# Kernel tuning notes

Measured on AMD Instinct MI355X. Metric: run time of the kernel, lower is better.

The kernel has to match this reference:

```python
import jax, jax.numpy as jnp
import numpy as np
import itertools

SKS = 3
GROUPS = 8
PAD = (SKS - 1) // 2


def setup_inputs() -> dict:
    key = jax.random.key(0)
    k1, k2 = jax.random.split(key)
    B, C, D, H, W = 2, 64, 64, 64, 64
    x = jax.random.normal(k1, (B, C, D, H, W), dtype=jnp.float32)
    w = jax.random.normal(k2, (B, GROUPS, SKS ** 3, D, H, W), dtype=jnp.float32)
    return {"x": x, "w": w}


def reference(x, w):
    # x: [B, C, D, H, W]; w: [B, G, sks^3, D, H, W]
    B, C, D, H, W = x.shape
    G = GROUPS
    # group the channels: [B, G, C//G, D, H, W]
    xg = x.reshape(B, G, C // G, D, H, W)
    offsets = list(itertools.product(range(-PAD, PAD + 1), repeat=3))  # (di, hi, wi), 27 taps
    out = jnp.zeros_like(xg)
    for k, (di, hi, wi) in enumerate(offsets):
        # circular shift matching torch.roll(x_g, (-di,-hi,-wi), dims=(2,3,4))
        shifted = jnp.roll(xg, shift=(-di, -hi, -wi), axis=(3, 4, 5))
        # broadcast per-group dynamic weight over the C//G channels in the group
        out = out + shifted * w[:, :, k][:, :, None]  # [B,G,C//G,D,H,W]
    return out.reshape(B, C, D, H, W)
```

## Files before the change

kernel.cpp:

```cpp
#include <hip/hip_runtime.h>


#define ND 64
#define NH 64
#define NW 64
#define HW 4096
#define DHW 262144
#define CPG 8

typedef const __attribute__((address_space(1))) unsigned int* gp_as1;
typedef __attribute__((address_space(3))) unsigned int* lp_as3;

__global__ __launch_bounds__(64, 1) void ska3d_kernel(const float* __restrict__ x,
                                                      const float* __restrict__ w,
                                                      float* __restrict__ out) {
    __shared__ float lds[4][CPG][6][NW];

    const int lane = threadIdx.x;
    const int w0   = (lane & 15) * 4;
    const int hl   = lane >> 4;

    const int bid = blockIdx.x;
    const int dc  = bid & 7;
    const int ht  = (bid >> 3) & 15;
    const int g   = (bid >> 7) & 7;
    const int b   = bid >> 10;

    const int d0 = dc * 8;
    const int h0 = ht * 4;
    const int h  = h0 + hl;

    const float* xb = x + (size_t)(b * 64 + g * CPG) * DHW;
    const float* wb = w + (size_t)(b * 8 + g) * 27 * DHW;
    float* ob = out + (size_t)(b * 64 + g * CPG) * DHW + h * NW + w0;

    const int wlb = (w0 + 60) & 63;
    const int wrb = (w0 + 4) & 63;

#define STAGE(p) do {                                                          \
        const int slot_ = (p) & 3;                                             \
        const int dd_   = (p) & 63;                                            \
        _Pragma("unroll")                                                      \
        for (int i = 0; i < 12; ++i) {                                         \
            const int fid = i * 64 + lane;            \
            const int c_  = fid / 96;               \
            const int rm_ = fid - c_ * 96;                                     \
            const int r_  = rm_ >> 4;                                \
            const int ws_ = rm_ & 15;                               \
            const int hh_ = (h0 - 1 + r_) & 63;                                \
            const float* gsrc = xb + (size_t)c_ * DHW + dd_ * HW + hh_ * NW + ws_ * 4; \
            __builtin_amdgcn_global_load_lds((gp_as1)gsrc,                     \
                (lp_as3)&lds[slot_][c_][r_][ws_ * 4], 16, 0, 0);               \
        }                                                                      \
    } while (0)

    STAGE(d0 - 1);
    STAGE(d0);
    STAGE(d0 + 1);
    asm volatile("s_waitcnt vmcnt(0)" ::: "memory");

    for (int d = d0; d < d0 + 8; ++d) {
        STAGE(d + 2);

        float4 wk[27];
        const float* wpd = wb + (size_t)d * HW + h * NW + w0;
#pragma unroll
        for (int k = 0; k < 27; ++k)
            wk[k] = *(const float4*)(wpd + (size_t)k * DHW);

        asm volatile("s_waitcnt vmcnt(47)" ::: "memory");

        float acc[CPG][4];
#pragma unroll
        for (int c = 0; c < CPG; ++c)
            acc[c][0] = acc[c][1] = acc[c][2] = acc[c][3] = 0.f;

#pragma unroll
        for (int di = -1; di <= 1; ++di) {
            const int slot = (d + di) & 3;
#pragma unroll
            for (int hi = -1; hi <= 1; ++hi) {
                const int r  = hl + hi + 1;
                const int kb = (di + 1) * 9 + (hi + 1) * 3;
#pragma unroll
                for (int c = 0; c < CPG; ++c) {
                    const float* row = &lds[slot][c][r][0];
                    const float4 xm = *(const float4*)(row + wlb);
                    const float4 xv = *(const float4*)(row + w0);
                    const float4 xp = *(const float4*)(row + wrb);
                    const float4 wa = wk[kb], wm = wk[kb + 1], wc = wk[kb + 2];
                    acc[c][0] += wa.x * xm.w;  acc[c][1] += wa.y * xv.x;
                    acc[c][2] += wa.z * xv.y;  acc[c][3] += wa.w * xv.z;
                    acc[c][0] += wm.x * xv.x;  acc[c][1] += wm.y * xv.y;
                    acc[c][2] += wm.z * xv.z;  acc[c][3] += wm.w * xv.w;
                    acc[c][0] += wc.x * xv.y;  acc[c][1] += wc.y * xv.z;
                    acc[c][2] += wc.z * xv.w;  acc[c][3] += wc.w * xp.x;
                }
            }
        }

#pragma unroll
        for (int c = 0; c < CPG; ++c)
            *(float4*)(ob + (size_t)c * DHW + (size_t)d * HW) =
                make_float4(acc[c][0], acc[c][1], acc[c][2], acc[c][3]);
    }
}

extern "C" void kernel_launch(void* const* d_in, const int* in_sizes, int n_in,
                              void* d_out, int out_size, void* d_ws, size_t ws_size,
                              hipStream_t stream) {
    const float* x = (const float*)d_in[0];
    const float* w = (const float*)d_in[1];
    float* out = (float*)d_out;
    dim3 grid(2048);
    dim3 block(64);
    hipLaunchKernelGGL(ska3d_kernel, grid, block, 0, stream, x, w, out);
}
```

Baseline: 178.6 us.

## Double-buffer per-depth weight loads one slice ahead and shrink halo LDS reads

The depth loop is unrolled with two register sets for the 27 weight float4s. The weights for slice d+1 are issued while slice d is computed, so global weight latency overlaps with the FMA work instead of stalling at the start of each iteration. The left and right halo reads from LDS become single scalar loads instead of float4 loads, which cuts LDS traffic. In exchange, register pressure roughly doubles for the weights, and the manual vmcnt accounting becomes more fragile.

```diff
diff --git a/kernel.cpp b/kernel.cpp
--- a/kernel.cpp
+++ b/kernel.cpp
@@ -31,11 +31,11 @@
     const int h  = h0 + hl;
 
     const float* xb = x + (size_t)(b * 64 + g * CPG) * DHW;
-    const float* wb = w + (size_t)(b * 8 + g) * 27 * DHW;
+    const float* wb = w + (size_t)(b * 8 + g) * 27 * DHW + h * NW + w0;
     float* ob = out + (size_t)(b * 64 + g * CPG) * DHW + h * NW + w0;
 
-    const int wlb = (w0 + 60) & 63;
-    const int wrb = (w0 + 4) & 63;
+    const int wl = (w0 + 63) & 63;
+    const int wr = (w0 + 4) & 63;
 
 #define STAGE(p) do {                                                          \
         const int slot_ = (p) & 3;                                             \
@@ -43,7 +43,7 @@
         _Pragma("unroll")                                                      \
         for (int i = 0; i < 12; ++i) {                                         \
             const int fid = i * 64 + lane;            \
-            const int c_  = fid / 96;               \
+            const int c_  = fid / 96;                                          \
             const int rm_ = fid - c_ * 96;                                     \
             const int r_  = rm_ >> 4;                                \
             const int ws_ = rm_ & 15;                               \
@@ -54,56 +54,71 @@
         }                                                                      \
     } while (0)
 
+#define LOADW(arr, dp) do {                                                    \
+        const float* wpn_ = wb + (size_t)(dp) * HW;                            \
+        _Pragma("unroll")                                                      \
+        for (int k = 0; k < 27; ++k)                                           \
+            arr[k] = *(const float4*)(wpn_ + (size_t)k * DHW);                 \
+    } while (0)
+
+#define COMPUTE(d, WK) do {                                                    \
+        float acc[CPG][4];                                                     \
+        _Pragma("unroll")                                                      \
+        for (int c = 0; c < CPG; ++c)                                          \
+            acc[c][0] = acc[c][1] = acc[c][2] = acc[c][3] = 0.f;               \
+        _Pragma("unroll")                                                      \
+        for (int di = -1; di <= 1; ++di) {                                     \
+            const int slot = ((d) + di) & 3;                                   \
+            _Pragma("unroll")                                                  \
+            for (int hi = -1; hi <= 1; ++hi) {                                 \
+                const int r  = hl + hi + 1;                                    \
+                const int kb = (di + 1) * 9 + (hi + 1) * 3;                    \
+                _Pragma("unroll")                                              \
+                for (int c = 0; c < CPG; ++c) {                                \
+                    const float* row = &lds[slot][c][r][0];                    \
+                    const float  xm = row[wl];                                 \
+                    const float4 xv = *(const float4*)(row + w0);              \
+                    const float  xp = row[wr];                                 \
+                    const float4 wa = WK[kb], wm = WK[kb + 1], wc = WK[kb + 2];\
+                    acc[c][0] += wa.x * xm;    acc[c][1] += wa.y * xv.x;       \
+                    acc[c][2] += wa.z * xv.y;  acc[c][3] += wa.w * xv.z;       \
+                    acc[c][0] += wm.x * xv.x;  acc[c][1] += wm.y * xv.y;       \
+                    acc[c][2] += wm.z * xv.z;  acc[c][3] += wm.w * xv.w;       \
+                    acc[c][0] += wc.x * xv.y;  acc[c][1] += wc.y * xv.z;       \
+                    acc[c][2] += wc.z * xv.w;  acc[c][3] += wc.w * xp;         \
+                }                                                              \
+            }                                                                  \
+        }                                                                      \
+        _Pragma("unroll")                                                      \
+        for (int c = 0; c < CPG; ++c)                                          \
+            *(float4*)(ob + (size_t)c * DHW + (size_t)(d) * HW) =              \
+                make_float4(acc[c][0], acc[c][1], acc[c][2], acc[c][3]);       \
+    } while (0)
+
+#define BODY(d, WC, WN) do {                                                   \
+        STAGE((d) + 2);                                                        \
+        LOADW(WN, (d) + 1);                                                    \
+        asm volatile("s_waitcnt vmcnt(47)" ::: "memory");                      \
+        COMPUTE((d), WC);                                                      \
+    } while (0)
+
+    float4 wkA[27], wkB[27];
+
     STAGE(d0 - 1);
     STAGE(d0);
     STAGE(d0 + 1);
+    LOADW(wkA, d0);
     asm volatile("s_waitcnt vmcnt(0)" ::: "memory");
 
-    for (int d = d0; d < d0 + 8; ++d) {
-        STAGE(d + 2);
+#pragma unroll
+    for (int i = 0; i < 3; ++i) {
+        BODY(d0 + 2 * i,     wkA, wkB);
+        BODY(d0 + 2 * i + 1, wkB, wkA);
+    }
+    BODY(d0 + 6, wkA, wkB);
 
-        float4 wk[27];
-        const float* wpd = wb + (size_t)d * HW + h * NW + w0;
-#pragma unroll
-        for (int k = 0; k < 27; ++k)
-            wk[k] = *(const float4*)(wpd + (size_t)k * DHW);
-
-        asm volatile("s_waitcnt vmcnt(47)" ::: "memory");
-
-        float acc[CPG][4];
-#pragma unroll
-        for (int c = 0; c < CPG; ++c)
-            acc[c][0] = acc[c][1] = acc[c][2] = acc[c][3] = 0.f;
-
-#pragma unroll
-        for (int di = -1; di <= 1; ++di) {
-            const int slot = (d + di) & 3;
-#pragma unroll
-            for (int hi = -1; hi <= 1; ++hi) {
-                const int r  = hl + hi + 1;
-                const int kb = (di + 1) * 9 + (hi + 1) * 3;
-#pragma unroll
-                for (int c = 0; c < CPG; ++c) {
-                    const float* row = &lds[slot][c][r][0];
-                    const float4 xm = *(const float4*)(row + wlb);
-                    const float4 xv = *(const float4*)(row + w0);
-                    const float4 xp = *(const float4*)(row + wrb);
-                    const float4 wa = wk[kb], wm = wk[kb + 1], wc = wk[kb + 2];
-                    acc[c][0] += wa.x * xm.w;  acc[c][1] += wa.y * xv.x;
-                    acc[c][2] += wa.z * xv.y;  acc[c][3] += wa.w * xv.z;
-                    acc[c][0] += wm.x * xv.x;  acc[c][1] += wm.y * xv.y;
-                    acc[c][2] += wm.z * xv.z;  acc[c][3] += wm.w * xv.w;
-                    acc[c][0] += wc.x * xv.y;  acc[c][1] += wc.y * xv.z;
-                    acc[c][2] += wc.z * xv.w;  acc[c][3] += wc.w * xp.x;
-                }
-            }
-        }
-
-#pragma unroll
-        for (int c = 0; c < CPG; ++c)
-            *(float4*)(ob + (size_t)c * DHW + (size_t)d * HW) =
-                make_float4(acc[c][0], acc[c][1], acc[c][2], acc[c][3]);
-    }
+    asm volatile("s_waitcnt vmcnt(8)" ::: "memory");
+    COMPUTE(d0 + 7, wkB);
 }
 
 extern "C" void kernel_launch(void* const* d_in, const int* in_sizes, int n_in,
```

Result: slower. 182.3 us (+2.1%).

## Split group channels across four waves per block and prefetch next-depth weights

Applied to the files above, without the earlier changes.

Each block grows from one wave to four. Each wave computes two of the group's eight channels, and the three LDS halo planes are staged cooperatively, with an explicit s_waitcnt plus s_barrier per depth step. The 27 dynamic-weight vectors for the next depth slice are now loaded right after the current slice's stores, so their latency overlaps the next barrier and staging instead of sitting in front of the compute. The aim is more waves in flight to hide memory latency, and fewer registers per wave. In exchange, all four waves fetch the same weights, so per-block weight requests rise four-fold and depend on cache hits, and the new barrier adds a sync cost.

```diff
diff --git a/kernel.cpp b/kernel.cpp
--- a/kernel.cpp
+++ b/kernel.cpp
@@ -6,19 +6,21 @@
 #define NW 64
 #define HW 4096
 #define DHW 262144
-#define CPG 8
 
 typedef const __attribute__((address_space(1))) unsigned int* gp_as1;
 typedef __attribute__((address_space(3))) unsigned int* lp_as3;
 
-__global__ __launch_bounds__(64, 1) void ska3d_kernel(const float* __restrict__ x,
-                                                      const float* __restrict__ w,
-                                                      float* __restrict__ out) {
-    __shared__ float lds[4][CPG][6][NW];
+__global__ __launch_bounds__(256, 2) void ska3d_kernel(const float* __restrict__ x,
+                                                       const float* __restrict__ w,
+                                                       float* __restrict__ out) {
+    __shared__ float lds[4][8][6][NW];
 
-    const int lane = threadIdx.x;
+    const int tid  = threadIdx.x;
+    const int lane = tid & 63;
+    const int wv   = tid >> 6;
     const int w0   = (lane & 15) * 4;
     const int hl   = lane >> 4;
+    const int c0   = wv * 2;
 
     const int bid = blockIdx.x;
     const int dc  = bid & 7;
@@ -30,20 +32,20 @@
     const int h0 = ht * 4;
     const int h  = h0 + hl;
 
-    const float* xb = x + (size_t)(b * 64 + g * CPG) * DHW;
-    const float* wb = w + (size_t)(b * 8 + g) * 27 * DHW;
-    float* ob = out + (size_t)(b * 64 + g * CPG) * DHW + h * NW + w0;
+    const float* xb = x + (size_t)(b * 64 + g * 8) * DHW;
+    const float* wb = w + (size_t)(b * 8 + g) * 27 * DHW + h * NW + w0;
+    float* ob = out + (size_t)(b * 64 + g * 8 + c0) * DHW + h * NW + w0;
 
-    const int wlb = (w0 + 60) & 63;
-    const int wrb = (w0 + 4) & 63;
+    const int wl = (w0 + 63) & 63;
+    const int wr = (w0 + 4) & 63;
 
 #define STAGE(p) do {                                                          \
         const int slot_ = (p) & 3;                                             \
         const int dd_   = (p) & 63;                                            \
         _Pragma("unroll")                                                      \
-        for (int i = 0; i < 12; ++i) {                                         \
-            const int fid = i * 64 + lane;            \
-            const int c_  = fid / 96;               \
+        for (int i = 0; i < 3; ++i) {                                          \
+            const int fid = i * 256 + tid;                         \
+            const int c_  = fid / 96;                                          \
             const int rm_ = fid - c_ * 96;                                     \
             const int r_  = rm_ >> 4;                                \
             const int ws_ = rm_ & 15;                               \
@@ -54,26 +56,34 @@
         }                                                                      \
     } while (0)
 
+#define LOADW(dp) do {                                                         \
+        const float* wpn_ = wb + (size_t)(dp) * HW;                            \
+        _Pragma("unroll")                                                      \
+        for (int k = 0; k < 27; ++k)                                           \
+            wk[k] = *(const float4*)(wpn_ + (size_t)k * DHW);                  \
+    } while (0)
+
+    float4 wk[27];
+
     STAGE(d0 - 1);
     STAGE(d0);
     STAGE(d0 + 1);
+    LOADW(d0);
     asm volatile("s_waitcnt vmcnt(0)" ::: "memory");
 
-    for (int d = d0; d < d0 + 8; ++d) {
-        STAGE(d + 2);
+#pragma unroll 1
+    for (int i = 0; i < 8; ++i) {
+        const int d = d0 + i;
 
-        float4 wk[27];
-        const float* wpd = wb + (size_t)d * HW + h * NW + w0;
+        asm volatile("s_waitcnt vmcnt(29)" ::: "memory");
+        asm volatile("s_barrier" ::: "memory");
+
+        if (i < 7) STAGE(d + 2);
+
+        float acc[2][4];
 #pragma unroll
-        for (int k = 0; k < 27; ++k)
-            wk[k] = *(const float4*)(wpd + (size_t)k * DHW);
-
-        asm volatile("s_waitcnt vmcnt(47)" ::: "memory");
-
-        float acc[CPG][4];
-#pragma unroll
-        for (int c = 0; c < CPG; ++c)
-            acc[c][0] = acc[c][1] = acc[c][2] = acc[c][3] = 0.f;
+        for (int cc = 0; cc < 2; ++cc)
+            acc[cc][0] = acc[cc][1] = acc[cc][2] = acc[cc][3] = 0.f;
 
 #pragma unroll
         for (int di = -1; di <= 1; ++di) {
@@ -83,26 +93,28 @@
                 const int r  = hl + hi + 1;
                 const int kb = (di + 1) * 9 + (hi + 1) * 3;
 #pragma unroll
-                for (int c = 0; c < CPG; ++c) {
-                    const float* row = &lds[slot][c][r][0];
-                    const float4 xm = *(const float4*)(row + wlb);
+                for (int cc = 0; cc < 2; ++cc) {
+                    const float* row = &lds[slot][c0 + cc][r][0];
+                    const float  xm = row[wl];
                     const float4 xv = *(const float4*)(row + w0);
-                    const float4 xp = *(const float4*)(row + wrb);
+                    const float  xp = row[wr];
                     const float4 wa = wk[kb], wm = wk[kb + 1], wc = wk[kb + 2];
-                    acc[c][0] += wa.x * xm.w;  acc[c][1] += wa.y * xv.x;
-                    acc[c][2] += wa.z * xv.y;  acc[c][3] += wa.w * xv.z;
-                    acc[c][0] += wm.x * xv.x;  acc[c][1] += wm.y * xv.y;
-                    acc[c][2] += wm.z * xv.z;  acc[c][3] += wm.w * xv.w;
-                    acc[c][0] += wc.x * xv.y;  acc[c][1] += wc.y * xv.z;
-                    acc[c][2] += wc.z * xv.w;  acc[c][3] += wc.w * xp.x;
+                    acc[cc][0] += wa.x * xm;    acc[cc][1] += wa.y * xv.x;
+                    acc[cc][2] += wa.z * xv.y;  acc[cc][3] += wa.w * xv.z;
+                    acc[cc][0] += wm.x * xv.x;  acc[cc][1] += wm.y * xv.y;
+                    acc[cc][2] += wm.z * xv.z;  acc[cc][3] += wm.w * xv.w;
+                    acc[cc][0] += wc.x * xv.y;  acc[cc][1] += wc.y * xv.z;
+                    acc[cc][2] += wc.z * xv.w;  acc[cc][3] += wc.w * xp;
                 }
             }
         }
 
 #pragma unroll
-        for (int c = 0; c < CPG; ++c)
-            *(float4*)(ob + (size_t)c * DHW + (size_t)d * HW) =
-                make_float4(acc[c][0], acc[c][1], acc[c][2], acc[c][3]);
+        for (int cc = 0; cc < 2; ++cc)
+            *(float4*)(ob + (size_t)cc * DHW + (size_t)d * HW) =
+                make_float4(acc[cc][0], acc[cc][1], acc[cc][2], acc[cc][3]);
+
+        if (i < 7) LOADW(d + 1);
     }
 }
 
@@ -113,6 +125,6 @@
     const float* w = (const float*)d_in[1];
     float* out = (float*)d_out;
     dim3 grid(2048);
-    dim3 block(64);
+    dim3 block(256);
     hipLaunchKernelGGL(ska3d_kernel, grid, block, 0, stream, x, w, out);
 }
```

Measured after the change: 170.0 us. 4.8% less time.
